# Optimization experiments

Hardware: AMD Instinct MI355X
Metric: run time of the kernel (lower is better)

The kernel has to match this reference:

```python
import jax, jax.numpy as jnp
import numpy as np

# Canonical Mamba-1 block dims
D_MODEL = 1024
D_INNER = 2048        # d_model * projection_size (expand=2)
D_STATE = 16          # SSM state size N (Mamba default)
DT_RANK = 64          # d_model // 16 (Mamba default)
KER = 4               # conv_ker
BATCH, SEQ = 2, 1024


def setup_inputs() -> dict:
    key = jax.random.key(0)
    ks = jax.random.split(key, 8)
    sc = lambda k, shape, s: (jax.random.normal(k, shape, dtype=jnp.float32) * s)
    A_log = jnp.log(jnp.broadcast_to(
        jnp.arange(1, D_STATE + 1, dtype=jnp.float32), (D_INNER, D_STATE)))
    return {
        "hidden_states": jax.random.normal(ks[0], (BATCH, SEQ, D_MODEL), dtype=jnp.float32),
        "in_proj_w": sc(ks[1], (D_MODEL, 2 * D_INNER), 0.02),
        "conv_w": sc(ks[2], (D_INNER, 1, KER), 0.1),      # depthwise conv kernel [O, I/groups=1, K]
        "conv_b": jnp.zeros((D_INNER,), dtype=jnp.float32),
        "x_proj_w": sc(ks[3], (D_INNER, DT_RANK + 2 * D_STATE), 0.02),
        "dt_proj_w": sc(ks[4], (DT_RANK, D_INNER), 0.05),
        "dt_proj_b": jnp.full((D_INNER,), -4.6, dtype=jnp.float32),  # softplus(-4.6) ~ 0.01 init dt
        "A_log": A_log,
        "D_skip": jnp.ones((D_INNER,), dtype=jnp.float32),
        "out_proj_w": sc(ks[5], (D_INNER, D_MODEL), 0.02),
    }


def _selective_scan(u, delta, A, Bm, Cm, D_skip):
    """u, delta: [B,L,D]; A: [D,N]; Bm, Cm: [B,L,N]; D_skip: [D]."""
    # Discretize: seq-major for lax.scan
    dA = jnp.exp(jnp.einsum('bld,dn->lbdn', delta, A))            # [L,B,D,N]
    dBu = jnp.einsum('bld,bln,bld->lbdn', delta, Bm, u)           # [L,B,D,N]

    def step(h, ab):
        dA_t, dBu_t = ab
        h = dA_t * h + dBu_t
        return h, h

    h0 = jnp.zeros((u.shape[0], A.shape[0], A.shape[1]), u.dtype)  # [B,D,N]
    _, hs = jax.lax.scan(step, h0, (dA, dBu))                      # hs: [L,B,D,N]
    y = jnp.einsum('lbdn,bln->bld', hs, Cm)
    return y + u * D_skip


def reference(hidden_states, in_proj_w, conv_w, conv_b, x_proj_w,
              dt_proj_w, dt_proj_b, A_log, D_skip, out_proj_w):
    silu = jax.nn.silu
    # Input projection -> (x, res), each [B,L,D_INNER]
    xz = hidden_states @ in_proj_w
    x, res = jnp.split(xz, 2, axis=-1)

    # Causal depthwise conv over sequence: [B,D,L] layout
    x_c = jnp.transpose(x, (0, 2, 1))
    x_c = jax.lax.conv_general_dilated(
        x_c, conv_w, window_strides=(1,), padding=[(KER - 1, 0)],
        dimension_numbers=('NCH', 'OIH', 'NCH'), feature_group_count=D_INNER)
    x_c = x_c + conv_b[None, :, None]
    x = silu(jnp.transpose(x_c, (0, 2, 1)))                        # [B,L,D_INNER]

    # SSM parameterization
    x_dbl = x @ x_proj_w                                           # [B,L,dt_rank+2N]
    dt, Bm, Cm = jnp.split(x_dbl, [DT_RANK, DT_RANK + D_STATE], axis=-1)
    delta = jax.nn.softplus(dt @ dt_proj_w + dt_proj_b)            # [B,L,D_INNER]
    A = -jnp.exp(A_log)                                            # [D_INNER, N]

    y = _selective_scan(x, delta, A, Bm, Cm, D_skip)

    # SiLU gate and output projection
    y = y * silu(res)
    return y @ out_proj_w
```

## Files before the change

### kernel.cpp

```cpp
#include <hip/hip_runtime.h>
#include <hip/hip_bf16.h>
#include <cstdint>

#define D_MODEL  1024
#define D_INNER  2048
#define D_STATE  16
#define DT_RANK  64
#define KERW     4
#define BATCH    2
#define SEQ      1024
#define NTOK     (BATCH * SEQ)
#define CHUNKS   16
#define LC       (SEQ / CHUNKS)

typedef _Float16 h8 __attribute__((ext_vector_type(8)));
typedef _Float16 h4 __attribute__((ext_vector_type(4)));
typedef float    f32x4 __attribute__((ext_vector_type(4)));

__device__ __forceinline__ float siluf(float x) {
    return x / (1.f + __expf(-x));
}

#define GLOAD_LDS16(g, p) __builtin_amdgcn_global_load_lds( \
    (const __attribute__((address_space(1))) void*)(g),      \
    (__attribute__((address_space(3))) void*)(p), 16, 0, 0)

__global__ __launch_bounds__(256)
void f32_to_f16_k(const float* __restrict__ in, _Float16* __restrict__ out, int n4)
{
    int i = blockIdx.x * 256 + threadIdx.x;
    if (i >= n4) return;
    float4 v = ((const float4*)in)[i];
    h4 h = { (_Float16)v.x, (_Float16)v.y, (_Float16)v.z, (_Float16)v.w };
    *(h4*)(out + (size_t)i * 4) = h;
}

template<int NN>
__global__ __launch_bounds__(256)
void pack_b_f16(const float* __restrict__ B, _Float16* __restrict__ Bp, int K)
{
    constexpr int SH = (NN == 4096) ? 12 : 10;
    int gid = blockIdx.x * 256 + threadIdx.x;
    int n  = gid & (NN - 1);
    int kb = gid >> SH;
    h8 v;
    #pragma unroll
    for (int j = 0; j < 8; ++j)
        v[j] = (_Float16)B[(size_t)(kb * 8 + j) * NN + n];
    *(h8*)(Bp + (size_t)gid * 8) = v;
}

__global__ __launch_bounds__(256)
void gemm_f16_mfma(const _Float16* __restrict__ A, const _Float16* __restrict__ Bp,
                   float* __restrict__ C, int N, int K, int lda, int ldc)
{
    __shared__ alignas(16) _Float16 As[4 * 128 * 8];
    __shared__ alignas(16) _Float16 Bs[4 * 128 * 8];

    const int tid = threadIdx.x;
    const int l = tid & 63, w = tid >> 6;
    const int wm = w >> 1, wn = w & 1;
    const int bm = blockIdx.y * 128, bn = blockIdx.x * 128;

    f32x4 acc[4][4] = {};

    const int kg = l >> 4, r = l & 15;

    for (int k0 = 0; k0 < K; k0 += 32) {
        #pragma unroll
        for (int i = 0; i < 2; ++i) {
            int c = i * 256 + w * 64 + l;
            int row = c & 127, kgc = c >> 7;
            const _Float16* g = A + (size_t)(bm + row) * lda + k0 + kgc * 8;
            GLOAD_LDS16(g, As + (size_t)(i * 256 + w * 64) * 8);
        }
        #pragma unroll
        for (int i = 0; i < 2; ++i) {
            int c = i * 256 + w * 64 + l;
            int col = c & 127, kgc = c >> 7;
            const _Float16* g = Bp + ((size_t)((k0 >> 3) + kgc) * N + bn + col) * 8;
            GLOAD_LDS16(g, Bs + (size_t)(i * 256 + w * 64) * 8);
        }
        __syncthreads();

        h8 a[4], b[4];
        #pragma unroll
        for (int mi = 0; mi < 4; ++mi)
            a[mi] = *(const h8*)(As + (size_t)(kg * 128 + wm * 64 + mi * 16 + r) * 8);
        #pragma unroll
        for (int ni = 0; ni < 4; ++ni)
            b[ni] = *(const h8*)(Bs + (size_t)(kg * 128 + wn * 64 + ni * 16 + r) * 8);

        #pragma unroll
        for (int mi = 0; mi < 4; ++mi)
            #pragma unroll
            for (int ni = 0; ni < 4; ++ni)
                acc[mi][ni] = __builtin_amdgcn_mfma_f32_16x16x32_f16(
                    a[mi], b[ni], acc[mi][ni], 0, 0, 0);

        __syncthreads();
    }

    const int q = l >> 4;
    #pragma unroll
    for (int mi = 0; mi < 4; ++mi)
        #pragma unroll
        for (int ni = 0; ni < 4; ++ni)
            #pragma unroll
            for (int j = 0; j < 4; ++j)
                C[(size_t)(bm + wm * 64 + mi * 16 + q * 4 + j) * ldc
                  + (bn + wn * 64 + ni * 16 + r)] = acc[mi][ni][j];
}

template<bool BIAS, bool SOFTPLUS>
__global__ __launch_bounds__(256)
void gemm_f32(const float* __restrict__ A, const float* __restrict__ B,
              const float* __restrict__ bias, float* __restrict__ C,
              int M, int N, int K, int lda, int ldb, int ldc)
{
    __shared__ float As[16][68];
    __shared__ float Bs[16][68];
    const int tid = threadIdx.x;
    const int tx = tid & 15, ty = tid >> 4;
    const int bm = blockIdx.y * 64, bn = blockIdx.x * 64;

    float acc[4][4] = {};

    const int ar  = tid >> 2;
    const int ac4 = (tid & 3) << 2;
    const int bkr = tid >> 4;
    const int bc4 = (tid & 15) << 2;

    for (int k0 = 0; k0 < K; k0 += 16) {
        float4 av = make_float4(0.f, 0.f, 0.f, 0.f);
        {
            int row = bm + ar;
            if (row < M)
                av = *(const float4*)(A + (size_t)row * lda + (k0 + ac4));
        }
        As[ac4 + 0][ar] = av.x; As[ac4 + 1][ar] = av.y;
        As[ac4 + 2][ar] = av.z; As[ac4 + 3][ar] = av.w;

        float4 bv = make_float4(0.f, 0.f, 0.f, 0.f);
        {
            int col = bn + bc4;
            const float* bp = B + (size_t)(k0 + bkr) * ldb + col;
            if (col + 3 < N) {
                bv = *(const float4*)bp;
            } else {
                if (col + 0 < N) bv.x = bp[0];
                if (col + 1 < N) bv.y = bp[1];
                if (col + 2 < N) bv.z = bp[2];
                if (col + 3 < N) bv.w = bp[3];
            }
        }
        Bs[bkr][bc4 + 0] = bv.x; Bs[bkr][bc4 + 1] = bv.y;
        Bs[bkr][bc4 + 2] = bv.z; Bs[bkr][bc4 + 3] = bv.w;

        __syncthreads();

        #pragma unroll
        for (int kk = 0; kk < 16; ++kk) {
            float a[4], b[4];
            #pragma unroll
            for (int i = 0; i < 4; ++i) a[i] = As[kk][ty * 4 + i];
            #pragma unroll
            for (int j = 0; j < 4; ++j) b[j] = Bs[kk][tx * 4 + j];
            #pragma unroll
            for (int i = 0; i < 4; ++i)
                #pragma unroll
                for (int j = 0; j < 4; ++j)
                    acc[i][j] = fmaf(a[i], b[j], acc[i][j]);
        }
        __syncthreads();
    }

    #pragma unroll
    for (int i = 0; i < 4; ++i) {
        int row = bm + ty * 4 + i;
        if (row >= M) continue;
        #pragma unroll
        for (int j = 0; j < 4; ++j) {
            int col = bn + tx * 4 + j;
            if (col >= N) continue;
            float v = acc[i][j];
            if (BIAS) v += bias[col];
            if (SOFTPLUS) v = (v > 20.f) ? v : log1pf(__expf(v));
            C[(size_t)row * ldc + col] = v;
        }
    }
}

__global__ __launch_bounds__(256)
void gemm_f32_splitk(const float* __restrict__ A, const float* __restrict__ B,
                     float* __restrict__ part,
                     int M, int N, int K, int lda, int ldb, int ldc)
{
    __shared__ float As[16][68];
    __shared__ float Bs[16][68];
    const int tid = threadIdx.x;
    const int tx = tid & 15, ty = tid >> 4;
    const int bm = blockIdx.y * 64, bn = blockIdx.x * 64;
    const int kslice = K / gridDim.z;
    const int kbeg = blockIdx.z * kslice;

    float acc[4][4] = {};

    const int ar  = tid >> 2;
    const int ac4 = (tid & 3) << 2;
    const int bkr = tid >> 4;
    const int bc4 = (tid & 15) << 2;

    for (int k0 = kbeg; k0 < kbeg + kslice; k0 += 16) {
        float4 av;
        {
            int row = bm + ar;
            av = *(const float4*)(A + (size_t)row * lda + (k0 + ac4));
        }
        As[ac4 + 0][ar] = av.x; As[ac4 + 1][ar] = av.y;
        As[ac4 + 2][ar] = av.z; As[ac4 + 3][ar] = av.w;

        float4 bv = make_float4(0.f, 0.f, 0.f, 0.f);
        {
            int col = bn + bc4;
            const float* bp = B + (size_t)(k0 + bkr) * ldb + col;
            if (col + 3 < N) {
                bv = *(const float4*)bp;
            } else {
                if (col + 0 < N) bv.x = bp[0];
                if (col + 1 < N) bv.y = bp[1];
                if (col + 2 < N) bv.z = bp[2];
                if (col + 3 < N) bv.w = bp[3];
            }
        }
        Bs[bkr][bc4 + 0] = bv.x; Bs[bkr][bc4 + 1] = bv.y;
        Bs[bkr][bc4 + 2] = bv.z; Bs[bkr][bc4 + 3] = bv.w;

        __syncthreads();

        #pragma unroll
        for (int kk = 0; kk < 16; ++kk) {
            float a[4], b[4];
            #pragma unroll
            for (int i = 0; i < 4; ++i) a[i] = As[kk][ty * 4 + i];
            #pragma unroll
            for (int j = 0; j < 4; ++j) b[j] = Bs[kk][tx * 4 + j];
            #pragma unroll
            for (int i = 0; i < 4; ++i)
                #pragma unroll
                for (int j = 0; j < 4; ++j)
                    acc[i][j] = fmaf(a[i], b[j], acc[i][j]);
        }
        __syncthreads();
    }

    float* dst = part + (size_t)blockIdx.z * M * ldc;
    #pragma unroll
    for (int i = 0; i < 4; ++i) {
        int row = bm + ty * 4 + i;
        #pragma unroll
        for (int j = 0; j < 4; ++j) {
            int col = bn + tx * 4 + j;
            if (col >= N) continue;
            dst[(size_t)row * ldc + col] = acc[i][j];
        }
    }
}

__global__ __launch_bounds__(256)
void reduce_splitk(const float* __restrict__ part, float* __restrict__ out,
                   int n, int S)
{
    int i = blockIdx.x * 256 + threadIdx.x;
    if (i >= n) return;
    float s = 0.f;
    for (int j = 0; j < S; ++j) s += part[(size_t)j * n + i];
    out[i] = s;
}

__global__ __launch_bounds__(256)
void conv_silu(const float* __restrict__ xz, const float* __restrict__ conv_w,
               const float* __restrict__ conv_b, float* __restrict__ u)
{
    int idx = blockIdx.x * 256 + threadIdx.x;
    if (idx >= NTOK * D_INNER) return;
    int d = idx & (D_INNER - 1);
    int t = idx >> 11;
    int l = t & (SEQ - 1);
    int b = t >> 10;

    float w0 = conv_w[d * 4 + 0], w1 = conv_w[d * 4 + 1];
    float w2 = conv_w[d * 4 + 2], w3 = conv_w[d * 4 + 3];

    const float* base = xz + (size_t)b * SEQ * (2 * D_INNER) + d;
    float acc = conv_b[d];
    if (l >= 3) acc += w0 * base[(size_t)(l - 3) * (2 * D_INNER)];
    if (l >= 2) acc += w1 * base[(size_t)(l - 2) * (2 * D_INNER)];
    if (l >= 1) acc += w2 * base[(size_t)(l - 1) * (2 * D_INNER)];
    acc += w3 * base[(size_t)l * (2 * D_INNER)];

    u[idx] = siluf(acc);
}

__global__ __launch_bounds__(256)
void scan_pass1(const float* __restrict__ delta, const float* __restrict__ u,
                const float* __restrict__ xdbl, const float* __restrict__ A_log,
                float* __restrict__ Aprod, float* __restrict__ Hend)
{
    int t = blockIdx.x * 256 + threadIdx.x;
    if (t >= BATCH * CHUNKS * D_INNER) return;
    int d  = t & (D_INNER - 1);
    int bc = t >> 11;
    int c  = bc & (CHUNKS - 1);
    int b  = bc >> 4;

    float An[16];
    {
        const float4* a4 = (const float4*)(A_log + d * 16);
        #pragma unroll
        for (int q = 0; q < 4; ++q) {
            float4 v = a4[q];
            An[q * 4 + 0] = -__expf(v.x);
            An[q * 4 + 1] = -__expf(v.y);
            An[q * 4 + 2] = -__expf(v.z);
            An[q * 4 + 3] = -__expf(v.w);
        }
    }

    const float* dp = delta + ((size_t)b * SEQ + c * LC) * D_INNER + d;
    const float* up = u     + ((size_t)b * SEQ + c * LC) * D_INNER + d;
    const float* xb = xdbl  + ((size_t)b * SEQ + c * LC) * 96 + DT_RANK;

    float h[16], ap[16];
    #pragma unroll
    for (int n = 0; n < 16; ++n) { h[n] = 0.f; ap[n] = 1.f; }

    for (int l = 0; l < LC; ++l) {
        float dt = dp[(size_t)l * D_INNER];
        float ut = up[(size_t)l * D_INNER];
        const float4* b4 = (const float4*)(xb + l * 96);
        float4 B0 = b4[0], B1 = b4[1], B2 = b4[2], B3 = b4[3];
        float Bv[16] = { B0.x, B0.y, B0.z, B0.w, B1.x, B1.y, B1.z, B1.w,
                         B2.x, B2.y, B2.z, B2.w, B3.x, B3.y, B3.z, B3.w };
        float dtu = dt * ut;
        #pragma unroll
        for (int n = 0; n < 16; ++n) {
            float da = __expf(dt * An[n]);
            h[n]  = fmaf(da, h[n], dtu * Bv[n]);
            ap[n] *= da;
        }
    }

    float4* hp = (float4*)(Hend  + (size_t)t * 16);
    float4* pp = (float4*)(Aprod + (size_t)t * 16);
    #pragma unroll
    for (int q = 0; q < 4; ++q) {
        hp[q] = make_float4(h[q*4+0], h[q*4+1], h[q*4+2], h[q*4+3]);
        pp[q] = make_float4(ap[q*4+0], ap[q*4+1], ap[q*4+2], ap[q*4+3]);
    }
}

__global__ __launch_bounds__(256)
void scan_pass2(const float* __restrict__ Aprod, float* __restrict__ HendHin)
{
    int idx = blockIdx.x * 256 + threadIdx.x;
    if (idx >= BATCH * D_INNER * D_STATE) return;
    int n = idx & 15;
    int d = (idx >> 4) & (D_INNER - 1);
    int b = idx >> 15;

    float h = 0.f;
    for (int c = 0; c < CHUNKS; ++c) {
        size_t j = ((((size_t)b * CHUNKS + c) * D_INNER) + d) * 16 + n;
        float ap = Aprod[j];
        float he = HendHin[j];
        HendHin[j] = h;
        h = ap * h + he;
    }
}

__global__ __launch_bounds__(256)
void scan_pass3(const float* __restrict__ delta, const float* __restrict__ u,
                const float* __restrict__ xdbl, const float* __restrict__ xz,
                const float* __restrict__ A_log, const float* __restrict__ D_skip,
                const float* __restrict__ Hin, _Float16* __restrict__ ygh)
{
    int t = blockIdx.x * 256 + threadIdx.x;
    if (t >= BATCH * CHUNKS * D_INNER) return;
    int d  = t & (D_INNER - 1);
    int bc = t >> 11;
    int c  = bc & (CHUNKS - 1);
    int b  = bc >> 4;

    float An[16];
    {
        const float4* a4 = (const float4*)(A_log + d * 16);
        #pragma unroll
        for (int q = 0; q < 4; ++q) {
            float4 v = a4[q];
            An[q * 4 + 0] = -__expf(v.x);
            An[q * 4 + 1] = -__expf(v.y);
            An[q * 4 + 2] = -__expf(v.z);
            An[q * 4 + 3] = -__expf(v.w);
        }
    }
    float Dd = D_skip[d];

    float h[16];
    {
        const float4* h4p = (const float4*)(Hin + (size_t)t * 16);
        #pragma unroll
        for (int q = 0; q < 4; ++q) {
            float4 v = h4p[q];
            h[q * 4 + 0] = v.x; h[q * 4 + 1] = v.y;
            h[q * 4 + 2] = v.z; h[q * 4 + 3] = v.w;
        }
    }

    const float* dp = delta + ((size_t)b * SEQ + c * LC) * D_INNER + d;
    const float* up = u     + ((size_t)b * SEQ + c * LC) * D_INNER + d;
    const float* xb = xdbl  + ((size_t)b * SEQ + c * LC) * 96 + DT_RANK;
    const float* rp = xz    + ((size_t)b * SEQ + c * LC) * (2 * D_INNER) + D_INNER + d;
    _Float16*    yp = ygh   + ((size_t)b * SEQ + c * LC) * 8192 + d;

    for (int l = 0; l < LC; ++l) {
        float dt = dp[(size_t)l * D_INNER];
        float ut = up[(size_t)l * D_INNER];
        float res = rp[(size_t)l * (2 * D_INNER)];
        const float4* b4 = (const float4*)(xb + l * 96);
        float4 B0 = b4[0], B1 = b4[1], B2 = b4[2], B3 = b4[3];
        float4 C0 = b4[4], C1 = b4[5], C2 = b4[6], C3 = b4[7];
        float Bv[16] = { B0.x, B0.y, B0.z, B0.w, B1.x, B1.y, B1.z, B1.w,
                         B2.x, B2.y, B2.z, B2.w, B3.x, B3.y, B3.z, B3.w };
        float Cv[16] = { C0.x, C0.y, C0.z, C0.w, C1.x, C1.y, C1.z, C1.w,
                         C2.x, C2.y, C2.z, C2.w, C3.x, C3.y, C3.z, C3.w };
        float dtu = dt * ut;
        float y = 0.f;
        #pragma unroll
        for (int n = 0; n < 16; ++n) {
            float da = __expf(dt * An[n]);
            h[n] = fmaf(da, h[n], dtu * Bv[n]);
            y = fmaf(h[n], Cv[n], y);
        }
        yp[(size_t)l * 8192] = (_Float16)((y + ut * Dd) * siluf(res));
    }
}

extern "C" void kernel_launch(void* const* d_in, const int* in_sizes, int n_in,
                              void* d_out, int out_size, void* d_ws, size_t ws_size,
                              hipStream_t stream)
{
    const float* H      = (const float*)d_in[0];
    const float* Win    = (const float*)d_in[1];
    const float* convw  = (const float*)d_in[2];
    const float* convb  = (const float*)d_in[3];
    const float* xprojw = (const float*)d_in[4];
    const float* dtw    = (const float*)d_in[5];
    const float* dtb    = (const float*)d_in[6];
    const float* Alog   = (const float*)d_in[7];
    const float* Dskip  = (const float*)d_in[8];
    const float* Wout   = (const float*)d_in[9];
    float* out = (float*)d_out;

    float* ws    = (float*)d_ws;
    float* xz    = ws;
    float* u     = xz   + (size_t)NTOK * 4096;
    float* xdbl  = u    + (size_t)NTOK * 2048;
    float* delta = xdbl + (size_t)NTOK * 96;
    float* Aprod = delta + (size_t)NTOK * 2048;
    float* Hend  = Aprod + (size_t)BATCH * CHUNKS * D_INNER * 16;

    _Float16* Hh    = (_Float16*)delta;
    _Float16* Winp  = (_Float16*)delta + 2 * 1024 * 1024;
    float*    part  = delta;
    _Float16* ygh   = (_Float16*)xz;
    _Float16* Woutp = (_Float16*)Aprod;

    dim3 blk(256);

    f32_to_f16_k<<<(NTOK * D_MODEL / 4) / 256, blk, 0, stream>>>(H, Hh, NTOK * D_MODEL / 4);
    pack_b_f16<4096><<<((D_MODEL / 8) * 4096) / 256, blk, 0, stream>>>(Win, Winp, D_MODEL);

    gemm_f16_mfma<<<dim3(4096 / 128, NTOK / 128), blk, 0, stream>>>(
        Hh, Winp, xz, 2 * D_INNER, D_MODEL, D_MODEL, 2 * D_INNER);

    conv_silu<<<(NTOK * D_INNER) / 256, blk, 0, stream>>>(xz, convw, convb, u);

    gemm_f32_splitk<<<dim3(2, NTOK / 64, 16), blk, 0, stream>>>(
        u, xprojw, part, NTOK, 96, D_INNER, D_INNER, 96, 96);
    reduce_splitk<<<(NTOK * 96 + 255) / 256, blk, 0, stream>>>(
        part, xdbl, NTOK * 96, 16);

    gemm_f32<true, true><<<dim3(D_INNER / 64, NTOK / 64), blk, 0, stream>>>(
        xdbl, dtw, dtb, delta, NTOK, D_INNER, DT_RANK, 96, D_INNER, D_INNER);

    {
        int nthr = BATCH * CHUNKS * D_INNER;
        scan_pass1<<<nthr / 256, blk, 0, stream>>>(delta, u, xdbl, Alog, Aprod, Hend);
        scan_pass2<<<(BATCH * D_INNER * 16) / 256, blk, 0, stream>>>(Aprod, Hend);
        scan_pass3<<<nthr / 256, blk, 0, stream>>>(delta, u, xdbl, xz, Alog, Dskip,
                                                   Hend , ygh);
    }

    pack_b_f16<1024><<<((D_INNER / 8) * 1024) / 256, blk, 0, stream>>>(Wout, Woutp, D_INNER);

    gemm_f16_mfma<<<dim3(1024 / 128, NTOK / 128), blk, 0, stream>>>(
        ygh, Woutp, out, D_MODEL, D_INNER, 8192, D_MODEL);
}
```

Baseline: 347.7 us.

## Double-buffer MFMA GEMM, shrink N tile, swizzle blocks, split-K out_proj

Reworks the f16 MFMA GEMM to double-buffer its LDS tiles, so global-to-LDS loads for the next K step overlap the MFMAs on the current one. The N tile shrinks from 128 to 64 to launch more workgroups, and a 1D grid is remapped with an XCD-style interleave. The output projection is split along K into two slices written to a workspace and summed by a reduce kernel. The aims are better latency hiding and higher occupancy. The cost is less reuse per tile, more blocks, and an extra reduction pass over the out_proj result.

```diff
diff --git a/kernel.cpp b/kernel.cpp
--- a/kernel.cpp
+++ b/kernel.cpp
@@ -50,66 +50,87 @@
     *(h8*)(Bp + (size_t)gid * 8) = v;
 }
 
+__device__ __forceinline__ void stage_tiles(
+    const _Float16* __restrict__ A, const _Float16* __restrict__ Bp,
+    _Float16* as, _Float16* bs, int bm, int bn, int k0, int N, int lda, int tid)
+{
+    #pragma unroll
+    for (int i = 0; i < 2; ++i) {
+        int c = i * 256 + tid;
+        int row = c & 127, kgc = c >> 7;
+        const _Float16* g = A + (size_t)(bm + row) * lda + k0 + kgc * 8;
+        GLOAD_LDS16(g, as + (size_t)c * 8);
+    }
+    {
+        int c = tid;
+        int col = c & 63, kgc = c >> 6;
+        const _Float16* g = Bp + ((size_t)((k0 >> 3) + kgc) * N + bn + col) * 8;
+        GLOAD_LDS16(g, bs + (size_t)c * 8);
+    }
+}
+
 __global__ __launch_bounds__(256)
 void gemm_f16_mfma(const _Float16* __restrict__ A, const _Float16* __restrict__ Bp,
-                   float* __restrict__ C, int N, int K, int lda, int ldc)
-{
-    __shared__ alignas(16) _Float16 As[4 * 128 * 8];
-    __shared__ alignas(16) _Float16 Bs[4 * 128 * 8];
+                   float* __restrict__ C, int M, int N, int K, int lda, int ldc)
+{
+    __shared__ alignas(16) _Float16 As[2][4 * 128 * 8];
+    __shared__ alignas(16) _Float16 Bs[2][4 * 64 * 8];
 
     const int tid = threadIdx.x;
     const int l = tid & 63, w = tid >> 6;
     const int wm = w >> 1, wn = w & 1;
-    const int bm = blockIdx.y * 128, bn = blockIdx.x * 128;
-
-    f32x4 acc[4][4] = {};
-
+
+    const int nwg = gridDim.x;
+    const int qch = nwg >> 3;
+    const int wg  = ((blockIdx.x & 7) * qch) + (blockIdx.x >> 3);
+    const int nbn = N >> 6;
+    const int bn  = (wg % nbn) * 64;
+    const int bm  = (wg / nbn) * 128;
+
+    const int kslice = K / gridDim.z;
+    const int kbeg = blockIdx.z * kslice;
+    const int kend = kbeg + kslice;
+
+    f32x4 acc[4][2] = {};
     const int kg = l >> 4, r = l & 15;
 
-    for (int k0 = 0; k0 < K; k0 += 32) {
-        #pragma unroll
-        for (int i = 0; i < 2; ++i) {
-            int c = i * 256 + w * 64 + l;
-            int row = c & 127, kgc = c >> 7;
-            const _Float16* g = A + (size_t)(bm + row) * lda + k0 + kgc * 8;
-            GLOAD_LDS16(g, As + (size_t)(i * 256 + w * 64) * 8);
-        }
-        #pragma unroll
-        for (int i = 0; i < 2; ++i) {
-            int c = i * 256 + w * 64 + l;
-            int col = c & 127, kgc = c >> 7;
-            const _Float16* g = Bp + ((size_t)((k0 >> 3) + kgc) * N + bn + col) * 8;
-            GLOAD_LDS16(g, Bs + (size_t)(i * 256 + w * 64) * 8);
-        }
-        __syncthreads();
-
-        h8 a[4], b[4];
+    stage_tiles(A, Bp, As[0], Bs[0], bm, bn, kbeg, N, lda, tid);
+    __syncthreads();
+
+    int cur = 0;
+    for (int k0 = kbeg; k0 < kend; k0 += 32) {
+        if (k0 + 32 < kend)
+            stage_tiles(A, Bp, As[cur ^ 1], Bs[cur ^ 1], bm, bn, k0 + 32, N, lda, tid);
+
+        h8 a[4], b[2];
         #pragma unroll
         for (int mi = 0; mi < 4; ++mi)
-            a[mi] = *(const h8*)(As + (size_t)(kg * 128 + wm * 64 + mi * 16 + r) * 8);
-        #pragma unroll
-        for (int ni = 0; ni < 4; ++ni)
-            b[ni] = *(const h8*)(Bs + (size_t)(kg * 128 + wn * 64 + ni * 16 + r) * 8);
+            a[mi] = *(const h8*)(As[cur] + (size_t)(kg * 128 + wm * 64 + mi * 16 + r) * 8);
+        #pragma unroll
+        for (int ni = 0; ni < 2; ++ni)
+            b[ni] = *(const h8*)(Bs[cur] + (size_t)(kg * 64 + wn * 32 + ni * 16 + r) * 8);
 
         #pragma unroll
         for (int mi = 0; mi < 4; ++mi)
             #pragma unroll
-            for (int ni = 0; ni < 4; ++ni)
+            for (int ni = 0; ni < 2; ++ni)
                 acc[mi][ni] = __builtin_amdgcn_mfma_f32_16x16x32_f16(
                     a[mi], b[ni], acc[mi][ni], 0, 0, 0);
 
         __syncthreads();
-    }
-
+        cur ^= 1;
+    }
+
+    float* dst = C + (size_t)blockIdx.z * M * ldc;
     const int q = l >> 4;
     #pragma unroll
     for (int mi = 0; mi < 4; ++mi)
         #pragma unroll
-        for (int ni = 0; ni < 4; ++ni)
+        for (int ni = 0; ni < 2; ++ni)
             #pragma unroll
             for (int j = 0; j < 4; ++j)
-                C[(size_t)(bm + wm * 64 + mi * 16 + q * 4 + j) * ldc
-                  + (bn + wn * 64 + ni * 16 + r)] = acc[mi][ni][j];
+                dst[(size_t)(bm + wm * 64 + mi * 16 + q * 4 + j) * ldc
+                    + (bn + wn * 32 + ni * 16 + r)] = acc[mi][ni][j];
 }
 
 template<bool BIAS, bool SOFTPLUS>
@@ -473,6 +494,7 @@
     _Float16* Hh    = (_Float16*)delta;
     _Float16* Winp  = (_Float16*)delta + 2 * 1024 * 1024;
     float*    part  = delta;
+    float*    part4 = delta;
     _Float16* ygh   = (_Float16*)xz;
     _Float16* Woutp = (_Float16*)Aprod;
 
@@ -481,8 +503,8 @@
     f32_to_f16_k<<<(NTOK * D_MODEL / 4) / 256, blk, 0, stream>>>(H, Hh, NTOK * D_MODEL / 4);
     pack_b_f16<4096><<<((D_MODEL / 8) * 4096) / 256, blk, 0, stream>>>(Win, Winp, D_MODEL);
 
-    gemm_f16_mfma<<<dim3(4096 / 128, NTOK / 128), blk, 0, stream>>>(
-        Hh, Winp, xz, 2 * D_INNER, D_MODEL, D_MODEL, 2 * D_INNER);
+    gemm_f16_mfma<<<dim3((4096 / 64) * (NTOK / 128), 1, 1), blk, 0, stream>>>(
+        Hh, Winp, xz, NTOK, 2 * D_INNER, D_MODEL, D_MODEL, 2 * D_INNER);
 
     conv_silu<<<(NTOK * D_INNER) / 256, blk, 0, stream>>>(xz, convw, convb, u);
 
@@ -504,6 +526,8 @@
 
     pack_b_f16<1024><<<((D_INNER / 8) * 1024) / 256, blk, 0, stream>>>(Wout, Woutp, D_INNER);
 
-    gemm_f16_mfma<<<dim3(1024 / 128, NTOK / 128), blk, 0, stream>>>(
-        ygh, Woutp, out, D_MODEL, D_INNER, 8192, D_MODEL);
-}
+    gemm_f16_mfma<<<dim3((1024 / 64) * (NTOK / 128), 1, 2), blk, 0, stream>>>(
+        ygh, Woutp, part4, NTOK, D_MODEL, D_INNER, 8192, D_MODEL);
+    reduce_splitk<<<(NTOK * D_MODEL) / 256, blk, 0, stream>>>(
+        part4, out, NTOK * D_MODEL, 2);
+}
```

Measured after the change: 333.1 us. 1.04x faster.
